# Performance work log

Measured on AMD Instinct MI355X. Metric: run time of the kernel, lower is better.

## Reference

```python
import jax, jax.numpy as jnp
import numpy as np

N_EMBED = 1024
NUM_HEADS = 16
HEAD_SIZE = 64  # NUM_HEADS * HEAD_SIZE == N_EMBED
BLOCK_SIZE = 2048


def setup_inputs() -> dict:
    key = jax.random.key(0)
    ks = jax.random.split(key, 9)
    s = 1.0 / np.sqrt(N_EMBED)
    batch_x = jax.random.normal(ks[0], (4, BLOCK_SIZE, N_EMBED), dtype=jnp.float32)
    # stacked per-head linear params: weight [H, E, d], bias [H, d]
    Wq = jax.random.uniform(ks[1], (NUM_HEADS, N_EMBED, HEAD_SIZE), jnp.float32, -s, s)
    Wk = jax.random.uniform(ks[2], (NUM_HEADS, N_EMBED, HEAD_SIZE), jnp.float32, -s, s)
    Wv = jax.random.uniform(ks[3], (NUM_HEADS, N_EMBED, HEAD_SIZE), jnp.float32, -s, s)
    bq = jax.random.uniform(ks[4], (NUM_HEADS, HEAD_SIZE), jnp.float32, -s, s)
    bk = jax.random.uniform(ks[5], (NUM_HEADS, HEAD_SIZE), jnp.float32, -s, s)
    bv = jax.random.uniform(ks[6], (NUM_HEADS, HEAD_SIZE), jnp.float32, -s, s)
    Wp = jax.random.uniform(ks[7], (N_EMBED, N_EMBED), jnp.float32, -s, s)
    bp = jax.random.uniform(ks[8], (N_EMBED,), jnp.float32, -s, s)
    return {"batch_x": batch_x, "Wq": Wq, "Wk": Wk, "Wv": Wv,
            "bq": bq, "bk": bk, "bv": bv, "Wp": Wp, "bp": bp}


def reference(batch_x, Wq, Wk, Wv, bq, bk, bv, Wp, bp):
    B, T, E = batch_x.shape
    # per-head projections: [B, H, T, d]
    q = jnp.einsum('bte,hed->bhtd', batch_x, Wq) + bq[None, :, None, :]
    k = jnp.einsum('bte,hed->bhtd', batch_x, Wk) + bk[None, :, None, :]
    v = jnp.einsum('bte,hed->bhtd', batch_x, Wv) + bv[None, :, None, :]
    scale = 1.0 / jnp.sqrt(jnp.asarray(HEAD_SIZE, batch_x.dtype))
    wei = jnp.einsum('bhtd,bhsd->bhts', q, k) * scale  # [B,H,T,T]
    causal = jnp.tril(jnp.ones((T, T), dtype=bool))
    wei = jnp.where(causal, wei, jnp.asarray(-jnp.inf, wei.dtype))
    wei = jax.nn.softmax(wei, axis=-1)
    out = jnp.einsum('bhts,bhsd->bhtd', wei, v)  # [B,H,T,d]
    # concat heads (head order matches torch.cat over ModuleList)
    out = out.transpose(0, 2, 1, 3).reshape(B, T, NUM_HEADS * HEAD_SIZE)
    return out @ Wp + bp
```

## Files before the change

### kernel.cpp

```cpp
#include <hip/hip_runtime.h>
#include <math.h>

#define B_ 4
#define T_ 2048
#define E_ 1024
#define H_ 16
#define D_ 64

typedef __bf16 bf16_t;
typedef bf16_t bf16x8 __attribute__((ext_vector_type(8)));
typedef float  f32x4  __attribute__((ext_vector_type(4)));
typedef float  f32x16 __attribute__((ext_vector_type(16)));
typedef unsigned short u16x4 __attribute__((ext_vector_type(4)));
typedef unsigned int   u32x4 __attribute__((ext_vector_type(4)));

static __device__ __forceinline__ unsigned short f2bf(float f) {
    bf16_t h = (bf16_t)f;
    return __builtin_bit_cast(unsigned short, h);
}
static __device__ __forceinline__ unsigned int pk2(float a, float b) {
    return (unsigned int)f2bf(a) | ((unsigned int)f2bf(b) << 16);
}
static __device__ __forceinline__ float ex2(float x) {
    float r; asm("v_exp_f32 %0, %1" : "=v"(r) : "v"(x)); return r;
}
static __device__ __forceinline__ void pl32swap(unsigned int& a, unsigned int& b) {
    asm("v_permlane32_swap_b32 %0, %1" : "+v"(a), "+v"(b));
}

#define GLD(gp, lp) __builtin_amdgcn_global_load_lds( \
    (const __attribute__((address_space(1))) unsigned int*)(gp), \
    (__attribute__((address_space(3))) unsigned int*)(lp), 16, 0, 0)

#define BAR() __builtin_amdgcn_s_barrier()
#define WAIT_LGKM0() asm volatile("s_waitcnt lgkmcnt(0)" ::: "memory")

__global__ void cast_x_kernel(const float* __restrict__ in, unsigned short* __restrict__ out, int n4) {
    int i = blockIdx.x * blockDim.x + threadIdx.x;
    if (i >= n4) return;
    float4 v = ((const float4*)in)[i];
    ushort4 o;
    o.x = f2bf(v.x); o.y = f2bf(v.y); o.z = f2bf(v.z); o.w = f2bf(v.w);
    ((ushort4*)out)[i] = o;
}

__global__ void tcast_all(const float* __restrict__ Wq, const float* __restrict__ Wk,
                          const float* __restrict__ Wv, const float* __restrict__ Wp,
                          unsigned short* __restrict__ wf, unsigned short* __restrict__ wpt) {
    __shared__ unsigned short Ts[64 * 66];
    const int grp = blockIdx.y >> 4, yy = blockIdx.y & 15;
    const float* in; unsigned short* out; int yA, S;
    if (grp == 3) { in = Wp; out = wpt; yA = 64;    S = 1024; }
    else {
        in = (grp == 0) ? Wq : (grp == 1) ? Wk : Wv;
        out = wf + (size_t)grp * 1024 * 1024; yA = 65536; S = 64;
    }
    const int tid = threadIdx.x;
    const int r = tid >> 2, c4 = tid & 3;
    const float* ip = in + (size_t)yA * yy + (size_t)(blockIdx.x * 64 + r) * S + c4 * 16;
    #pragma unroll
    for (int j = 0; j < 4; ++j) {
        float4 v = *(const float4*)&ip[j * 4];
        Ts[(c4 * 16 + j * 4 + 0) * 66 + r] = f2bf(v.x);
        Ts[(c4 * 16 + j * 4 + 1) * 66 + r] = f2bf(v.y);
        Ts[(c4 * 16 + j * 4 + 2) * 66 + r] = f2bf(v.z);
        Ts[(c4 * 16 + j * 4 + 3) * 66 + r] = f2bf(v.w);
    }
    __syncthreads();
    unsigned short* op = out + (size_t)(yy * 64 + r) * 1024 + blockIdx.x * 64 + c4 * 16;
    #pragma unroll
    for (int j = 0; j < 4; ++j) {
        u16x4 pk;
        #pragma unroll
        for (int m = 0; m < 4; ++m) pk[m] = Ts[r * 66 + c4 * 16 + j * 4 + m];
        *(u16x4*)&op[j * 4] = pk;
    }
}

__global__ __launch_bounds__(512, 2) void qkv_gemm(
    const unsigned short* __restrict__ xb,
    const unsigned short* __restrict__ wf,
    const float* __restrict__ bq, const float* __restrict__ bk, const float* __restrict__ bv,
    unsigned short* __restrict__ qo, unsigned short* __restrict__ ko,
    unsigned short* __restrict__ vt)
{
    __shared__ __align__(16) unsigned short sm[65536];

    const int tid = threadIdx.x;
    const int w = tid >> 6, lane = tid & 63;
    const int wr = w >> 2, wc = w & 3;
    const int l15 = lane & 15, quad = lane >> 4, lsw = l15 & 7;
    const int m0 = blockIdx.x * 256;
    const int n0 = blockIdx.y * 256;

    f32x4 acc[8][4];
    #pragma unroll
    for (int i = 0; i < 8; ++i)
        #pragma unroll
        for (int j = 0; j < 4; ++j) acc[i][j] = (f32x4){0.f, 0.f, 0.f, 0.f};

    const int swzE = (((lane & 7) ^ (lane >> 3)) * 8);
    const unsigned short* Agb = xb + (size_t)(m0 + w * 16 + (lane >> 3)) * 1024 + swzE;
    const unsigned short* Bgb = wf + (size_t)(n0 + w * 16 + (lane >> 3)) * 1024 + swzE;

    auto stage_half = [&](int t, int which) {
        unsigned short* dst = sm + (t & 1) * 32768 + which * 8192 + w * 1024;
        const unsigned short* src = ((which < 2) ? Agb : Bgb)
                                  + (size_t)((which & 1) * 128) * 1024 + t * 64;
        GLD(src, dst);
        GLD(src + (size_t)8 * 1024, dst + 512);
    };
    auto rdA = [&](int t, int fm, int ks) {
        const int row = wr * 128 + fm * 16 + l15;
        return *(const bf16x8*)&sm[(t & 1) * 32768 + (row >> 7) * 8192
                                   + (row & 127) * 64 + (((ks * 4 + quad) ^ lsw) * 8)];
    };
    auto rdB = [&](int t, int fn, int ks) {
        const int row = wc * 64 + fn * 16 + l15;
        return *(const bf16x8*)&sm[(t & 1) * 32768 + 16384 + (row >> 7) * 8192
                                   + (row & 127) * 64 + (((ks * 4 + quad) ^ lsw) * 8)];
    };

    stage_half(0, 0); stage_half(0, 1); stage_half(0, 2); stage_half(0, 3);
    stage_half(1, 2); stage_half(1, 3);
    asm volatile("s_waitcnt vmcnt(4)" ::: "memory");
    BAR();

    #define MFMA_Q(mb, nb) \
        __builtin_amdgcn_s_setprio(1); \
        _Pragma("unroll") \
        for (int i_ = 0; i_ < 4; ++i_) \
            _Pragma("unroll") \
            for (int j_ = 0; j_ < 2; ++j_) \
                _Pragma("unroll") \
                for (int ks_ = 0; ks_ < 2; ++ks_) \
                    acc[(mb) + i_][(nb) + j_] = __builtin_amdgcn_mfma_f32_16x16x32_bf16( \
                        fA[i_][ks_], fB[(nb) + j_][ks_], acc[(mb) + i_][(nb) + j_], 0, 0, 0); \
        __builtin_amdgcn_s_setprio(0);

    #pragma unroll 1
    for (int it = 0; it < 8; ++it) {
        const int t0 = 2 * it, t1 = 2 * it + 1;
        const bool more = it < 7;
        bf16x8 fA[4][2], fB[4][2];

        #pragma unroll
        for (int m = 0; m < 4; ++m) { fA[m][0] = rdA(t0, m, 0); fA[m][1] = rdA(t0, m, 1); }
        #pragma unroll
        for (int n = 0; n < 2; ++n) { fB[n][0] = rdB(t0, n, 0); fB[n][1] = rdB(t0, n, 1); }
        stage_half(t1, 0);
        BAR(); WAIT_LGKM0();
        MFMA_Q(0, 0);
        BAR();

        #pragma unroll
        for (int n = 0; n < 2; ++n) { fB[2 + n][0] = rdB(t0, 2 + n, 0); fB[2 + n][1] = rdB(t0, 2 + n, 1); }
        stage_half(t1, 1);
        BAR(); WAIT_LGKM0();
        MFMA_Q(0, 2);
        BAR();

        #pragma unroll
        for (int m = 0; m < 4; ++m) { fA[m][0] = rdA(t0, 4 + m, 0); fA[m][1] = rdA(t0, 4 + m, 1); }
        if (more) stage_half(t0 + 2, 2);
        BAR(); WAIT_LGKM0();
        MFMA_Q(4, 2);
        BAR();

        if (more) {
            stage_half(t0 + 2, 3);
            asm volatile("s_waitcnt vmcnt(4)" ::: "memory");
        } else {
            asm volatile("s_waitcnt vmcnt(0)" ::: "memory");
        }
        BAR();
        MFMA_Q(4, 0);
        BAR();

        #pragma unroll
        for (int m = 0; m < 4; ++m) { fA[m][0] = rdA(t1, m, 0); fA[m][1] = rdA(t1, m, 1); }
        #pragma unroll
        for (int n = 0; n < 2; ++n) { fB[n][0] = rdB(t1, n, 0); fB[n][1] = rdB(t1, n, 1); }
        if (more) stage_half(t0 + 2, 0);
        BAR(); WAIT_LGKM0();
        MFMA_Q(0, 0);
        BAR();

        #pragma unroll
        for (int n = 0; n < 2; ++n) { fB[2 + n][0] = rdB(t1, 2 + n, 0); fB[2 + n][1] = rdB(t1, 2 + n, 1); }
        if (more) stage_half(t0 + 2, 1);
        BAR(); WAIT_LGKM0();
        MFMA_Q(0, 2);
        BAR();

        #pragma unroll
        for (int m = 0; m < 4; ++m) { fA[m][0] = rdA(t1, 4 + m, 0); fA[m][1] = rdA(t1, 4 + m, 1); }
        if (more) stage_half(t1 + 2, 2);
        BAR(); WAIT_LGKM0();
        MFMA_Q(4, 2);
        BAR();

        if (more) {
            stage_half(t1 + 2, 3);
            asm volatile("s_waitcnt vmcnt(4)" ::: "memory");
        } else {
            asm volatile("s_waitcnt vmcnt(0)" ::: "memory");
        }
        BAR();
        MFMA_Q(4, 0);
        BAR();
    }
    #undef MFMA_Q

    const int which = n0 >> 10;
    const int nb = n0 & 1023;
    if (which < 2) {
        const float* bias = which ? bk : bq;
        unsigned short* outp = which ? ko : qo;
        const float sc = which ? 1.f : 0.125f * 1.44269504088896f;
        #pragma unroll
        for (int fm = 0; fm < 8; ++fm)
            #pragma unroll
            for (int fn = 0; fn < 4; ++fn) {
                int colg = nb + wc * 64 + fn * 16 + l15;
                int h = colg >> 6, d = colg & 63;
                float bi = bias[colg];
                #pragma unroll
                for (int r = 0; r < 4; ++r) {
                    int row = m0 + wr * 128 + fm * 16 + quad * 4 + r;
                    int b = row >> 11, t = row & 2047;
                    outp[(((size_t)b * 16 + h) * 2048 + t) * 64 + d] = f2bf((acc[fm][fn][r] + bi) * sc);
                }
            }
    } else {
        const int b = m0 >> 11;
        for (int mh = 0; mh < 2; ++mh)
            for (int nh = 0; nh < 2; ++nh) {
                __syncthreads();
                if (wr == mh && (wc >> 1) == nh) {
                    const int cc = wc & 1;
                    #pragma unroll
                    for (int fm = 0; fm < 8; ++fm)
                        #pragma unroll
                        for (int fn = 0; fn < 4; ++fn) {
                            int colL = cc * 64 + fn * 16 + l15;
                            int colg = nb + nh * 128 + colL;
                            float bi = bv[colg];
                            u16x4 pk;
                            #pragma unroll
                            for (int r = 0; r < 4; ++r) pk[r] = f2bf(acc[fm][fn][r] + bi);
                            *(u16x4*)&sm[colL * 136 + fm * 16 + quad * 4] = pk;
                        }
                }
                __syncthreads();
                const int nl = tid >> 2, tq = tid & 3;
                const int colg = nb + nh * 128 + nl;
                const int h = colg >> 6, d = colg & 63;
                const int t0 = (m0 & 2047) + mh * 128;
                unsigned short* dst = vt + (((size_t)b * 16 + h) * 64 + d) * 2048 + t0 + tq * 32;
                #pragma unroll
                for (int j = 0; j < 4; ++j)
                    *(float4*)&dst[j * 8] = *(const float4*)&sm[nl * 136 + tq * 32 + j * 8];
            }
    }
}

__global__ __launch_bounds__(256, 2) void attn_kernel(
    const unsigned short* __restrict__ q, const unsigned short* __restrict__ k,
    const unsigned short* __restrict__ vt, unsigned short* __restrict__ att2)
{
    __shared__ __align__(16) unsigned short KV[2][2][8192];

    const int tid = threadIdx.x;
    const int w = tid >> 6, lane = tid & 63;
    const int l31 = lane & 31, h = lane >> 5;
    const int bh = blockIdx.x;
    const int rs = l31 & 7, rv = l31 & 15;

    const unsigned short* kb = k  + (size_t)bh * 2048 * 64;
    const unsigned short* vb = vt + (size_t)bh * 64 * 2048;

    const size_t kOff = (size_t)(32 * w + (lane >> 3)) * 64 + (size_t)(((lane & 7) ^ (lane >> 3)) * 8);
    const int vRow = lane >> 4, vc = lane & 15;
    size_t vOff[4];
    #pragma unroll
    for (int r = 0; r < 4; ++r)
        vOff[r] = (size_t)(16 * w + 4 * r + vRow) * 2048
                + (size_t)((vc ^ ((4 * r + vRow) & 15)) * 8);

    auto stage = [&](int jt, int buf) {
        unsigned short* dK = &KV[buf][0][w * 2048];
        unsigned short* dV = &KV[buf][1][w * 2048];
        const unsigned short* sK = kb + kOff + (size_t)jt * 8192;
        #pragma unroll
        for (int r = 0; r < 4; ++r) GLD(sK + r * 512, dK + r * 512);
        #pragma unroll
        for (int r = 0; r < 4; ++r) GLD(vb + vOff[r] + jt * 128, dV + r * 512);
    };

    for (int leg = 0; leg < 2; ++leg) {
        const int qtile = leg ? (15 - (int)blockIdx.y) : (int)blockIdx.y;
        const int qb0 = qtile * 128;
        const int qmin = qb0 + w * 32, qmax = qmin + 31;
        const int qg = qmin + l31;
        const int trips = qtile + 1;

        bf16x8 fQ[4];
        {
            const unsigned short* qp = q + ((size_t)bh * 2048 + qg) * 64 + h * 8;
            #pragma unroll
            for (int ks = 0; ks < 4; ++ks) fQ[ks] = *(const bf16x8*)&qp[ks * 16];
        }

        f32x16 Oa[2], Ob[2];
        #pragma unroll
        for (int nt = 0; nt < 2; ++nt)
            #pragma unroll
            for (int i = 0; i < 16; ++i) { Oa[nt][i] = 0.f; Ob[nt][i] = 0.f; }
        float lsum = 0.f;

        stage(0, 0);
        asm volatile("s_waitcnt vmcnt(0)" ::: "memory");
        BAR();

        for (int jt = 0; jt < trips; ++jt) {
            const int buf = jt & 1;
            if (jt + 1 < trips) stage(jt + 1, buf ^ 1);
            const unsigned short* Ks = KV[buf][0];
            const unsigned short* Vs = KV[buf][1];
            const int key0 = jt * 128;

            f32x16 S[4];
            #pragma unroll
            for (int kt = 0; kt < 4; ++kt)
                #pragma unroll
                for (int i = 0; i < 16; ++i) S[kt][i] = 0.f;
            __builtin_amdgcn_s_setprio(1);
            #pragma unroll
            for (int kt = 0; kt < 4; ++kt) {
                if (key0 + 32 * kt <= qmax) {
                    const int row = kt * 32 + l31;
                    #pragma unroll
                    for (int ks = 0; ks < 4; ++ks) {
                        bf16x8 aK = *(const bf16x8*)&Ks[row * 64 + (((2 * ks + h) ^ rs) * 8)];
                        S[kt] = __builtin_amdgcn_mfma_f32_32x32x16_bf16(aK, fQ[ks], S[kt], 0, 0, 0);
                    }
                }
            }
            __builtin_amdgcn_s_setprio(0);

            #pragma unroll
            for (int kt = 0; kt < 4; ++kt) {
                if (key0 + 32 * kt <= qmax) {
                    const bool nm = (key0 + 32 * kt + 31) > qmin;
                    unsigned int e0[4], e1[4];
                    float lst = 0.f;
                    #pragma unroll
                    for (int g = 0; g < 4; ++g) {
                        float p[4];
                        #pragma unroll
                        for (int r = 0; r < 4; ++r) {
                            float pv = ex2(S[kt][4 * g + r]);
                            if (nm) {
                                int key = key0 + kt * 32 + 8 * g + 4 * h + r;
                                if (key > qg) pv = 0.f;
                            }
                            p[r] = pv;
                        }
                        lst += (p[0] + p[1]) + (p[2] + p[3]);
                        e0[g] = pk2(p[0], p[1]);
                        e1[g] = pk2(p[2], p[3]);
                    }
                    lsum += lst;

                    __builtin_amdgcn_s_setprio(1);
                    #pragma unroll
                    for (int s = 0; s < 2; ++s) {
                        unsigned int a = e0[2 * s], b = e0[2 * s + 1];
                        pl32swap(a, b);
                        unsigned int c2 = e1[2 * s], d2 = e1[2 * s + 1];
                        pl32swap(c2, d2);
                        u32x4 t; t[0] = a; t[1] = c2; t[2] = b; t[3] = d2;
                        bf16x8 aP = __builtin_bit_cast(bf16x8, t);
                        const int cb = 4 * kt + 2 * s;
                        #pragma unroll
                        for (int nt = 0; nt < 2; ++nt) {
                            const int drow = nt * 32 + l31;
                            bf16x8 bV = *(const bf16x8*)&Vs[drow * 128 + (((cb + h) ^ rv) * 8)];
                            if (kt & 1)
                                Ob[nt] = __builtin_amdgcn_mfma_f32_32x32x16_bf16(aP, bV, Ob[nt], 0, 0, 0);
                            else
                                Oa[nt] = __builtin_amdgcn_mfma_f32_32x32x16_bf16(aP, bV, Oa[nt], 0, 0, 0);
                        }
                    }
                    __builtin_amdgcn_s_setprio(0);
                }
            }

            asm volatile("s_waitcnt vmcnt(0)" ::: "memory");
            BAR();
        }

        lsum += __shfl_xor(lsum, 32);
        const float inv = 1.f / lsum;

        unsigned short* ob = att2 + ((size_t)bh * 2048 + qmin) * 64;
        #pragma unroll
        for (int g = 0; g < 4; ++g)
            #pragma unroll
            for (int r = 0; r < 4; ++r) {
                const int qy = 8 * g + 4 * h + r;
                const float iv = __shfl(inv, qy);
                #pragma unroll
                for (int nt = 0; nt < 2; ++nt)
                    ob[(size_t)qy * 64 + nt * 32 + l31] =
                        f2bf((Oa[nt][4 * g + r] + Ob[nt][4 * g + r]) * iv);
            }
    }
}

__global__ __launch_bounds__(256) void proj_gemm(
    const unsigned short* __restrict__ A,
    const unsigned short* __restrict__ wpt,
    const float* __restrict__ bp,
    float* __restrict__ out)
{
    __shared__ __align__(16) unsigned short sm[16384];
    unsigned short* As = sm;
    unsigned short* Bs = sm + 8192;

    const int tid = threadIdx.x;
    const int w = tid >> 6, lane = tid & 63, l15 = lane & 15, quad = lane >> 4;
    const int m0 = blockIdx.x * 128;
    const int n0 = blockIdx.y * 128;

    f32x4 acc[2][8];
    #pragma unroll
    for (int s = 0; s < 2; ++s)
        #pragma unroll
        for (int n = 0; n < 8; ++n) acc[s][n] = (f32x4){0.f, 0.f, 0.f, 0.f};

    const unsigned short* Ag = A + (size_t)(m0 >> 11) * 16 * 131072
                                 + (size_t)((m0 & 2047) + 32 * w + (lane >> 3)) * 64 + (lane & 7) * 8;
    const unsigned short* Bg = wpt + (size_t)(n0 + 32 * w + (lane >> 3)) * 1024 + (lane & 7) * 8;
    unsigned short* Al = As + (32 * w) * 64;
    unsigned short* Bl = Bs + (32 * w) * 64;

    for (int k0 = 0; k0 < 1024; k0 += 64) {
        __syncthreads();
        const size_t aoff = (size_t)(k0 >> 6) * 131072;
        #pragma unroll
        for (int j = 0; j < 4; ++j) {
            GLD(Ag + aoff + (size_t)(8 * j) * 64, Al + (8 * j) * 64);
            GLD(Bg + (size_t)(8 * j) * 1024 + k0, Bl + (8 * j) * 64);
        }
        __syncthreads();
        #pragma unroll
        for (int ks = 0; ks < 2; ++ks) {
            bf16x8 a0 = *(const bf16x8*)&As[(32 * w + l15) * 64 + ks * 32 + quad * 8];
            bf16x8 a1 = *(const bf16x8*)&As[(32 * w + 16 + l15) * 64 + ks * 32 + quad * 8];
            #pragma unroll
            for (int n = 0; n < 8; ++n) {
                bf16x8 b = *(const bf16x8*)&Bs[(16 * n + l15) * 64 + ks * 32 + quad * 8];
                acc[0][n] = __builtin_amdgcn_mfma_f32_16x16x32_bf16(a0, b, acc[0][n], 0, 0, 0);
                acc[1][n] = __builtin_amdgcn_mfma_f32_16x16x32_bf16(a1, b, acc[1][n], 0, 0, 0);
            }
        }
    }

    #pragma unroll
    for (int s = 0; s < 2; ++s)
        #pragma unroll
        for (int n = 0; n < 8; ++n) {
            float bi = bp[n0 + 16 * n + l15];
            #pragma unroll
            for (int r = 0; r < 4; ++r) {
                int row = m0 + 32 * w + 16 * s + quad * 4 + r;
                out[(size_t)row * 1024 + n0 + 16 * n + l15] = acc[s][n][r] + bi;
            }
        }
}

extern "C" void kernel_launch(void* const* d_in, const int* in_sizes, int n_in,
                              void* d_out, int out_size, void* d_ws, size_t ws_size,
                              hipStream_t stream) {
    const float* x  = (const float*)d_in[0];
    const float* Wq = (const float*)d_in[1];
    const float* Wk = (const float*)d_in[2];
    const float* Wv = (const float*)d_in[3];
    const float* bq = (const float*)d_in[4];
    const float* bk = (const float*)d_in[5];
    const float* bv = (const float*)d_in[6];
    const float* Wp = (const float*)d_in[7];
    const float* bp = (const float*)d_in[8];
    float* out = (float*)d_out;

    const size_t nx = (size_t)B_ * T_ * E_;
    unsigned short* base = (unsigned short*)d_ws;
    unsigned short* xb  = base;
    unsigned short* qb  = xb + nx;
    unsigned short* kb  = qb + nx;
    unsigned short* vtb = kb + nx;
    unsigned short* atb = vtb + nx;
    unsigned short* wf  = atb + nx;
    unsigned short* wpt = wf + 3072 * 1024;

    cast_x_kernel<<<(int)(nx / 4 + 255) / 256, 256, 0, stream>>>(x, xb, (int)(nx / 4));
    tcast_all<<<dim3(16, 64), 256, 0, stream>>>(Wq, Wk, Wv, Wp, wf, wpt);
    qkv_gemm<<<dim3(32, 12), 512, 0, stream>>>(xb, wf, bq, bk, bv, qb, kb, vtb);
    attn_kernel<<<dim3(64, 8), 256, 0, stream>>>(qb, kb, vtb, atb);
    proj_gemm<<<dim3(64, 8), 256, 0, stream>>>(atb, wpt, bp, out);
}
```

Before: 269.6 us.

## Share pipelined 128x256 GEMM core across QKV and projection kernels with XCD-aware block remap

The QKV GEMM tile drops from 256x256 to 128x256, which doubles the grid to 768 blocks for better CU fill. It launches on a 1D grid whose block index is remapped so neighbouring tiles land on the same XCD. The projection GEMM is rewritten to use the same double-buffered, swizzled, global_load_lds pipelined core, replacing its simple synchronous loop with 128x128 tiles. The smaller QKV tile lowers arithmetic intensity per block, and the shared macro adds more vmcnt bookkeeping that must be correct.

```diff
diff --git a/kernel.cpp b/kernel.cpp
--- a/kernel.cpp
+++ b/kernel.cpp
@@ -34,6 +34,7 @@
 
 #define BAR() __builtin_amdgcn_s_barrier()
 #define WAIT_LGKM0() asm volatile("s_waitcnt lgkmcnt(0)" ::: "memory")
+#define VMC(n) asm volatile("s_waitcnt vmcnt(" #n ")" ::: "memory")
 
 __global__ void cast_x_kernel(const float* __restrict__ in, unsigned short* __restrict__ out, int n4) {
     int i = blockIdx.x * blockDim.x + threadIdx.x;
@@ -77,6 +78,69 @@
     }
 }
 
+
+#define GEMM_CORE_DECLS \
+    const int tid = threadIdx.x; \
+    const int w = tid >> 6, lane = tid & 63; \
+    const int wr = w >> 2, wc = w & 3; \
+    const int l15 = lane & 15, quad = lane >> 4, lsw = l15 & 7; \
+    const int rowg = lane >> 3; \
+    const int swz = ((lane & 7) ^ rowg) * 8; \
+    f32x4 acc[4][4]; \
+    _Pragma("unroll") for (int i_ = 0; i_ < 4; ++i_) \
+        _Pragma("unroll") for (int j_ = 0; j_ < 4; ++j_) \
+            acc[i_][j_] = (f32x4){0.f, 0.f, 0.f, 0.f};
+
+#define MFMA_P(nb) \
+    __builtin_amdgcn_s_setprio(1); \
+    _Pragma("unroll") for (int m_ = 0; m_ < 4; ++m_) \
+        _Pragma("unroll") for (int j_ = 0; j_ < 2; ++j_) \
+            _Pragma("unroll") for (int k_ = 0; k_ < 2; ++k_) \
+                acc[m_][(nb) + j_] = __builtin_amdgcn_mfma_f32_16x16x32_bf16( \
+                    fA[m_][k_], fB[(nb) + j_][k_], acc[m_][(nb) + j_], 0, 0, 0); \
+    __builtin_amdgcn_s_setprio(0);
+
+#define GEMM_K_LOOP \
+    stageA(0, 0); stageA(0, 1); stageB(0, 0, 0); stageB(0, 0, 1); \
+    stageB(0, 1, 0); stageB(0, 1, 1); \
+    stageA(1, 0); stageA(1, 1); stageB(1, 0, 0); stageB(1, 0, 1); \
+    VMC(6); BAR(); \
+    _Pragma("unroll 1") \
+    for (int it = 0; it < 8; ++it) { \
+        const int t0 = 2 * it, t1 = 2 * it + 1; \
+        const bool more = it < 7; \
+        bf16x8 fA[4][2], fB[4][2]; \
+         \
+        _Pragma("unroll") for (int m_ = 0; m_ < 4; ++m_) { fA[m_][0] = rdA(t0, m_, 0); fA[m_][1] = rdA(t0, m_, 1); } \
+        _Pragma("unroll") for (int n_ = 0; n_ < 2; ++n_) { fB[n_][0] = rdB(t0, n_, 0); fB[n_][1] = rdB(t0, n_, 1); } \
+        stageB(t1, 1, 0); stageB(t1, 1, 1); \
+        BAR(); WAIT_LGKM0(); \
+        MFMA_P(0); \
+        VMC(6); BAR(); \
+         \
+        _Pragma("unroll") for (int n_ = 0; n_ < 2; ++n_) { fB[2 + n_][0] = rdB(t0, 2 + n_, 0); fB[2 + n_][1] = rdB(t0, 2 + n_, 1); } \
+        if (more) { stageA(t0 + 2, 0); stageA(t0 + 2, 1); stageB(t0 + 2, 0, 0); stageB(t0 + 2, 0, 1); } \
+        BAR(); WAIT_LGKM0(); \
+        MFMA_P(2); \
+        if (more) { VMC(6); } else { VMC(2); } \
+        BAR(); \
+         \
+        _Pragma("unroll") for (int m_ = 0; m_ < 4; ++m_) { fA[m_][0] = rdA(t1, m_, 0); fA[m_][1] = rdA(t1, m_, 1); } \
+        _Pragma("unroll") for (int n_ = 0; n_ < 2; ++n_) { fB[n_][0] = rdB(t1, n_, 0); fB[n_][1] = rdB(t1, n_, 1); } \
+        if (more) { stageB(t0 + 2, 1, 0); stageB(t0 + 2, 1, 1); } \
+        BAR(); WAIT_LGKM0(); \
+        MFMA_P(0); \
+        if (more) { VMC(6); } else { VMC(0); } \
+        BAR(); \
+         \
+        _Pragma("unroll") for (int n_ = 0; n_ < 2; ++n_) { fB[2 + n_][0] = rdB(t1, 2 + n_, 0); fB[2 + n_][1] = rdB(t1, 2 + n_, 1); } \
+        if (more) { stageA(t1 + 2, 0); stageA(t1 + 2, 1); stageB(t1 + 2, 0, 0); stageB(t1 + 2, 0, 1); } \
+        BAR(); WAIT_LGKM0(); \
+        MFMA_P(2); \
+        if (more) { VMC(6); } \
+        BAR(); \
+    }
+
 __global__ __launch_bounds__(512, 2) void qkv_gemm(
     const unsigned short* __restrict__ xb,
     const unsigned short* __restrict__ wf,
@@ -84,133 +148,36 @@
     unsigned short* __restrict__ qo, unsigned short* __restrict__ ko,
     unsigned short* __restrict__ vt)
 {
-    __shared__ __align__(16) unsigned short sm[65536];
-
-    const int tid = threadIdx.x;
-    const int w = tid >> 6, lane = tid & 63;
-    const int wr = w >> 2, wc = w & 3;
-    const int l15 = lane & 15, quad = lane >> 4, lsw = l15 & 7;
-    const int m0 = blockIdx.x * 256;
-    const int n0 = blockIdx.y * 256;
-
-    f32x4 acc[8][4];
-    #pragma unroll
-    for (int i = 0; i < 8; ++i)
-        #pragma unroll
-        for (int j = 0; j < 4; ++j) acc[i][j] = (f32x4){0.f, 0.f, 0.f, 0.f};
-
-    const int swzE = (((lane & 7) ^ (lane >> 3)) * 8);
-    const unsigned short* Agb = xb + (size_t)(m0 + w * 16 + (lane >> 3)) * 1024 + swzE;
-    const unsigned short* Bgb = wf + (size_t)(n0 + w * 16 + (lane >> 3)) * 1024 + swzE;
-
-    auto stage_half = [&](int t, int which) {
-        unsigned short* dst = sm + (t & 1) * 32768 + which * 8192 + w * 1024;
-        const unsigned short* src = ((which < 2) ? Agb : Bgb)
-                                  + (size_t)((which & 1) * 128) * 1024 + t * 64;
-        GLD(src, dst);
-        GLD(src + (size_t)8 * 1024, dst + 512);
+    __shared__ __align__(16) unsigned short sm[49152];
+
+    const int bid = blockIdx.x;
+    const int logical = (bid & 7) * 96 + (bid >> 3);
+    const int m0 = (logical & 63) * 128;
+    const int n0 = (logical >> 6) * 256;
+
+    GEMM_CORE_DECLS
+
+    auto stageA = [&](int t, int g) {
+        const int rb = w * 16 + g * 8;
+        unsigned short* dst = sm + (t & 1) * 24576 + rb * 64;
+        GLD(xb + (size_t)(m0 + rb + rowg) * 1024 + t * 64 + swz, dst);
+    };
+    auto stageB = [&](int t, int R, int g) {
+        const int rb = w * 16 + g * 8;
+        const int ar0 = (rb >> 5) * 64 + R * 32 + (rb & 31);
+        unsigned short* dst = sm + (t & 1) * 24576 + 8192 + ar0 * 64;
+        GLD(wf + (size_t)(n0 + ar0 + rowg) * 1024 + t * 64 + swz, dst);
     };
     auto rdA = [&](int t, int fm, int ks) {
-        const int row = wr * 128 + fm * 16 + l15;
-        return *(const bf16x8*)&sm[(t & 1) * 32768 + (row >> 7) * 8192
-                                   + (row & 127) * 64 + (((ks * 4 + quad) ^ lsw) * 8)];
+        const int row = wr * 64 + fm * 16 + l15;
+        return *(const bf16x8*)&sm[(t & 1) * 24576 + row * 64 + (((ks * 4 + quad) ^ lsw) * 8)];
     };
     auto rdB = [&](int t, int fn, int ks) {
         const int row = wc * 64 + fn * 16 + l15;
-        return *(const bf16x8*)&sm[(t & 1) * 32768 + 16384 + (row >> 7) * 8192
-                                   + (row & 127) * 64 + (((ks * 4 + quad) ^ lsw) * 8)];
-    };
-
-    stage_half(0, 0); stage_half(0, 1); stage_half(0, 2); stage_half(0, 3);
-    stage_half(1, 2); stage_half(1, 3);
-    asm volatile("s_waitcnt vmcnt(4)" ::: "memory");
-    BAR();
-
-    #define MFMA_Q(mb, nb) \
-        __builtin_amdgcn_s_setprio(1); \
-        _Pragma("unroll") \
-        for (int i_ = 0; i_ < 4; ++i_) \
-            _Pragma("unroll") \
-            for (int j_ = 0; j_ < 2; ++j_) \
-                _Pragma("unroll") \
-                for (int ks_ = 0; ks_ < 2; ++ks_) \
-                    acc[(mb) + i_][(nb) + j_] = __builtin_amdgcn_mfma_f32_16x16x32_bf16( \
-                        fA[i_][ks_], fB[(nb) + j_][ks_], acc[(mb) + i_][(nb) + j_], 0, 0, 0); \
-        __builtin_amdgcn_s_setprio(0);
-
-    #pragma unroll 1
-    for (int it = 0; it < 8; ++it) {
-        const int t0 = 2 * it, t1 = 2 * it + 1;
-        const bool more = it < 7;
-        bf16x8 fA[4][2], fB[4][2];
-
-        #pragma unroll
-        for (int m = 0; m < 4; ++m) { fA[m][0] = rdA(t0, m, 0); fA[m][1] = rdA(t0, m, 1); }
-        #pragma unroll
-        for (int n = 0; n < 2; ++n) { fB[n][0] = rdB(t0, n, 0); fB[n][1] = rdB(t0, n, 1); }
-        stage_half(t1, 0);
-        BAR(); WAIT_LGKM0();
-        MFMA_Q(0, 0);
-        BAR();
-
-        #pragma unroll
-        for (int n = 0; n < 2; ++n) { fB[2 + n][0] = rdB(t0, 2 + n, 0); fB[2 + n][1] = rdB(t0, 2 + n, 1); }
-        stage_half(t1, 1);
-        BAR(); WAIT_LGKM0();
-        MFMA_Q(0, 2);
-        BAR();
-
-        #pragma unroll
-        for (int m = 0; m < 4; ++m) { fA[m][0] = rdA(t0, 4 + m, 0); fA[m][1] = rdA(t0, 4 + m, 1); }
-        if (more) stage_half(t0 + 2, 2);
-        BAR(); WAIT_LGKM0();
-        MFMA_Q(4, 2);
-        BAR();
-
-        if (more) {
-            stage_half(t0 + 2, 3);
-            asm volatile("s_waitcnt vmcnt(4)" ::: "memory");
-        } else {
-            asm volatile("s_waitcnt vmcnt(0)" ::: "memory");
-        }
-        BAR();
-        MFMA_Q(4, 0);
-        BAR();
-
-        #pragma unroll
-        for (int m = 0; m < 4; ++m) { fA[m][0] = rdA(t1, m, 0); fA[m][1] = rdA(t1, m, 1); }
-        #pragma unroll
-        for (int n = 0; n < 2; ++n) { fB[n][0] = rdB(t1, n, 0); fB[n][1] = rdB(t1, n, 1); }
-        if (more) stage_half(t0 + 2, 0);
-        BAR(); WAIT_LGKM0();
-        MFMA_Q(0, 0);
-        BAR();
-
-        #pragma unroll
-        for (int n = 0; n < 2; ++n) { fB[2 + n][0] = rdB(t1, 2 + n, 0); fB[2 + n][1] = rdB(t1, 2 + n, 1); }
-        if (more) stage_half(t0 + 2, 1);
-        BAR(); WAIT_LGKM0();
-        MFMA_Q(0, 2);
-        BAR();
-
-        #pragma unroll
-        for (int m = 0; m < 4; ++m) { fA[m][0] = rdA(t1, 4 + m, 0); fA[m][1] = rdA(t1, 4 + m, 1); }
-        if (more) stage_half(t1 + 2, 2);
-        BAR(); WAIT_LGKM0();
-        MFMA_Q(4, 2);
-        BAR();
-
-        if (more) {
-            stage_half(t1 + 2, 3);
-            asm volatile("s_waitcnt vmcnt(4)" ::: "memory");
-        } else {
-            asm volatile("s_waitcnt vmcnt(0)" ::: "memory");
-        }
-        BAR();
-        MFMA_Q(4, 0);
-        BAR();
-    }
-    #undef MFMA_Q
+        return *(const bf16x8*)&sm[(t & 1) * 24576 + 8192 + row * 64 + (((ks * 4 + quad) ^ lsw) * 8)];
+    };
+
+    GEMM_K_LOOP
 
     const int which = n0 >> 10;
     const int nb = n0 & 1023;
@@ -219,7 +186,7 @@
         unsigned short* outp = which ? ko : qo;
         const float sc = which ? 1.f : 0.125f * 1.44269504088896f;
         #pragma unroll
-        for (int fm = 0; fm < 8; ++fm)
+        for (int fm = 0; fm < 4; ++fm)
             #pragma unroll
             for (int fn = 0; fn < 4; ++fn) {
                 int colg = nb + wc * 64 + fn * 16 + l15;
@@ -227,42 +194,92 @@
                 float bi = bias[colg];
                 #pragma unroll
                 for (int r = 0; r < 4; ++r) {
-                    int row = m0 + wr * 128 + fm * 16 + quad * 4 + r;
+                    int row = m0 + wr * 64 + fm * 16 + quad * 4 + r;
                     int b = row >> 11, t = row & 2047;
                     outp[(((size_t)b * 16 + h) * 2048 + t) * 64 + d] = f2bf((acc[fm][fn][r] + bi) * sc);
                 }
             }
     } else {
-        const int b = m0 >> 11;
-        for (int mh = 0; mh < 2; ++mh)
-            for (int nh = 0; nh < 2; ++nh) {
-                __syncthreads();
-                if (wr == mh && (wc >> 1) == nh) {
-                    const int cc = wc & 1;
+        const int b = m0 >> 11, t0r = m0 & 2047;
+        for (int nh = 0; nh < 2; ++nh) {
+            __syncthreads();
+            if ((wc >> 1) == nh) {
+                const int cc = wc & 1;
+                #pragma unroll
+                for (int fm = 0; fm < 4; ++fm)
                     #pragma unroll
-                    for (int fm = 0; fm < 8; ++fm)
+                    for (int fn = 0; fn < 4; ++fn) {
+                        int colL = cc * 64 + fn * 16 + l15;
+                        int colg = nb + nh * 128 + colL;
+                        float bi = bv[colg];
+                        u16x4 pk;
                         #pragma unroll
-                        for (int fn = 0; fn < 4; ++fn) {
-                            int colL = cc * 64 + fn * 16 + l15;
-                            int colg = nb + nh * 128 + colL;
-                            float bi = bv[colg];
-                            u16x4 pk;
-                            #pragma unroll
-                            for (int r = 0; r < 4; ++r) pk[r] = f2bf(acc[fm][fn][r] + bi);
-                            *(u16x4*)&sm[colL * 136 + fm * 16 + quad * 4] = pk;
-                        }
-                }
-                __syncthreads();
-                const int nl = tid >> 2, tq = tid & 3;
-                const int colg = nb + nh * 128 + nl;
-                const int h = colg >> 6, d = colg & 63;
-                const int t0 = (m0 & 2047) + mh * 128;
-                unsigned short* dst = vt + (((size_t)b * 16 + h) * 64 + d) * 2048 + t0 + tq * 32;
-                #pragma unroll
-                for (int j = 0; j < 4; ++j)
-                    *(float4*)&dst[j * 8] = *(const float4*)&sm[nl * 136 + tq * 32 + j * 8];
-            }
-    }
+                        for (int r = 0; r < 4; ++r) pk[r] = f2bf(acc[fm][fn][r] + bi);
+                        *(u16x4*)&sm[colL * 136 + wr * 64 + fm * 16 + quad * 4] = pk;
+                    }
+            }
+            __syncthreads();
+            const int nl = tid >> 2, tq = tid & 3;
+            const int colg = nb + nh * 128 + nl;
+            const int h = colg >> 6, d = colg & 63;
+            unsigned short* dst = vt + (((size_t)b * 16 + h) * 64 + d) * 2048 + t0r + tq * 32;
+            #pragma unroll
+            for (int j = 0; j < 4; ++j)
+                *(float4*)&dst[j * 8] = *(const float4*)&sm[nl * 136 + tq * 32 + j * 8];
+        }
+    }
+}
+
+__global__ __launch_bounds__(512, 2) void proj_gemm(
+    const unsigned short* __restrict__ A,
+    const unsigned short* __restrict__ wpt,
+    const float* __restrict__ bp,
+    float* __restrict__ out)
+{
+    __shared__ __align__(16) unsigned short sm[49152];
+
+    const int bid = blockIdx.x;
+    const int logical = (bid & 7) * 32 + (bid >> 3);
+    const int m0 = (logical & 63) * 128;
+    const int n0 = (logical >> 6) * 256;
+
+    GEMM_CORE_DECLS
+
+    const unsigned short* Ab = A + (size_t)(m0 >> 11) * 16 * 131072 + (size_t)(m0 & 2047) * 64;
+    auto stageA = [&](int t, int g) {
+        const int rb = w * 16 + g * 8;
+        unsigned short* dst = sm + (t & 1) * 24576 + rb * 64;
+        GLD(Ab + (size_t)t * 131072 + (rb + rowg) * 64 + swz, dst);
+    };
+    auto stageB = [&](int t, int R, int g) {
+        const int rb = w * 16 + g * 8;
+        const int ar0 = (rb >> 5) * 64 + R * 32 + (rb & 31);
+        unsigned short* dst = sm + (t & 1) * 24576 + 8192 + ar0 * 64;
+        GLD(wpt + (size_t)(n0 + ar0 + rowg) * 1024 + t * 64 + swz, dst);
+    };
+    auto rdA = [&](int t, int fm, int ks) {
+        const int row = wr * 64 + fm * 16 + l15;
+        return *(const bf16x8*)&sm[(t & 1) * 24576 + row * 64 + (((ks * 4 + quad) ^ lsw) * 8)];
+    };
+    auto rdB = [&](int t, int fn, int ks) {
+        const int row = wc * 64 + fn * 16 + l15;
+        return *(const bf16x8*)&sm[(t & 1) * 24576 + 8192 + row * 64 + (((ks * 4 + quad) ^ lsw) * 8)];
+    };
+
+    GEMM_K_LOOP
+
+    #pragma unroll
+    for (int fm = 0; fm < 4; ++fm)
+        #pragma unroll
+        for (int fn = 0; fn < 4; ++fn) {
+            int col = n0 + wc * 64 + fn * 16 + l15;
+            float bi = bp[col];
+            #pragma unroll
+            for (int r = 0; r < 4; ++r) {
+                int row = m0 + wr * 64 + fm * 16 + quad * 4 + r;
+                out[(size_t)row * 1024 + col] = acc[fm][fn][r] + bi;
+            }
+        }
 }
 
 __global__ __launch_bounds__(256, 2) void attn_kernel(
@@ -320,7 +337,7 @@
         float lsum = 0.f;
 
         stage(0, 0);
-        asm volatile("s_waitcnt vmcnt(0)" ::: "memory");
+        VMC(0);
         BAR();
 
         for (int jt = 0; jt < trips; ++jt) {
@@ -397,7 +414,7 @@
                 }
             }
 
-            asm volatile("s_waitcnt vmcnt(0)" ::: "memory");
+            VMC(0);
             BAR();
         }
 
@@ -417,68 +434,6 @@
                         f2bf((Oa[nt][4 * g + r] + Ob[nt][4 * g + r]) * iv);
             }
     }
-}
-
-__global__ __launch_bounds__(256) void proj_gemm(
-    const unsigned short* __restrict__ A,
-    const unsigned short* __restrict__ wpt,
-    const float* __restrict__ bp,
-    float* __restrict__ out)
-{
-    __shared__ __align__(16) unsigned short sm[16384];
-    unsigned short* As = sm;
-    unsigned short* Bs = sm + 8192;
-
-    const int tid = threadIdx.x;
-    const int w = tid >> 6, lane = tid & 63, l15 = lane & 15, quad = lane >> 4;
-    const int m0 = blockIdx.x * 128;
-    const int n0 = blockIdx.y * 128;
-
-    f32x4 acc[2][8];
-    #pragma unroll
-    for (int s = 0; s < 2; ++s)
-        #pragma unroll
-        for (int n = 0; n < 8; ++n) acc[s][n] = (f32x4){0.f, 0.f, 0.f, 0.f};
-
-    const unsigned short* Ag = A + (size_t)(m0 >> 11) * 16 * 131072
-                                 + (size_t)((m0 & 2047) + 32 * w + (lane >> 3)) * 64 + (lane & 7) * 8;
-    const unsigned short* Bg = wpt + (size_t)(n0 + 32 * w + (lane >> 3)) * 1024 + (lane & 7) * 8;
-    unsigned short* Al = As + (32 * w) * 64;
-    unsigned short* Bl = Bs + (32 * w) * 64;
-
-    for (int k0 = 0; k0 < 1024; k0 += 64) {
-        __syncthreads();
-        const size_t aoff = (size_t)(k0 >> 6) * 131072;
-        #pragma unroll
-        for (int j = 0; j < 4; ++j) {
-            GLD(Ag + aoff + (size_t)(8 * j) * 64, Al + (8 * j) * 64);
-            GLD(Bg + (size_t)(8 * j) * 1024 + k0, Bl + (8 * j) * 64);
-        }
-        __syncthreads();
-        #pragma unroll
-        for (int ks = 0; ks < 2; ++ks) {
-            bf16x8 a0 = *(const bf16x8*)&As[(32 * w + l15) * 64 + ks * 32 + quad * 8];
-            bf16x8 a1 = *(const bf16x8*)&As[(32 * w + 16 + l15) * 64 + ks * 32 + quad * 8];
-            #pragma unroll
-            for (int n = 0; n < 8; ++n) {
-                bf16x8 b = *(const bf16x8*)&Bs[(16 * n + l15) * 64 + ks * 32 + quad * 8];
-                acc[0][n] = __builtin_amdgcn_mfma_f32_16x16x32_bf16(a0, b, acc[0][n], 0, 0, 0);
-                acc[1][n] = __builtin_amdgcn_mfma_f32_16x16x32_bf16(a1, b, acc[1][n], 0, 0, 0);
-            }
-        }
-    }
-
-    #pragma unroll
-    for (int s = 0; s < 2; ++s)
-        #pragma unroll
-        for (int n = 0; n < 8; ++n) {
-            float bi = bp[n0 + 16 * n + l15];
-            #pragma unroll
-            for (int r = 0; r < 4; ++r) {
-                int row = m0 + 32 * w + 16 * s + quad * 4 + r;
-                out[(size_t)row * 1024 + n0 + 16 * n + l15] = acc[s][n][r] + bi;
-            }
-        }
 }
 
 extern "C" void kernel_launch(void* const* d_in, const int* in_sizes, int n_in,
@@ -507,7 +462,7 @@
 
     cast_x_kernel<<<(int)(nx / 4 + 255) / 256, 256, 0, stream>>>(x, xb, (int)(nx / 4));
     tcast_all<<<dim3(16, 64), 256, 0, stream>>>(Wq, Wk, Wv, Wp, wf, wpt);
-    qkv_gemm<<<dim3(32, 12), 512, 0, stream>>>(xb, wf, bq, bk, bv, qb, kb, vtb);
+    qkv_gemm<<<768, 512, 0, stream>>>(xb, wf, bq, bk, bv, qb, kb, vtb);
     attn_kernel<<<dim3(64, 8), 256, 0, stream>>>(qb, kb, vtb, atb);
-    proj_gemm<<<dim3(64, 8), 256, 0, stream>>>(atb, wpt, bp, out);
-}
+    proj_gemm<<<256, 512, 0, stream>>>(atb, wpt, bp, out);
+}
```

Result: no change. 265.6 us (-1.5%).
